# Optimization experiments

Measured on AMD Instinct MI355X. Metric: run time of the kernel, lower is better.

## Reference

```python
import math
import jax, jax.numpy as jnp
import numpy as np

WINDOW = (2, 7, 7)
SHIFT = (1, 3, 3)
NUM_HEADS = 4
DIM = 128
B, D, H, W = 1, 16, 112, 112  # divisible by window -> no padding, shift active


def _rel_coords_table():
    wd, wh, ww = WINDOW
    cd = np.arange(-(wd - 1), wd, dtype=np.float32)
    ch = np.arange(-(wh - 1), wh, dtype=np.float32)
    cw = np.arange(-(ww - 1), ww, dtype=np.float32)
    t = np.stack(np.meshgrid(cd, ch, cw, indexing='ij'), axis=-1)  # [2wd-1,2wh-1,2ww-1,3]
    t[..., 0] /= (wd - 1)
    t[..., 1] /= (wh - 1)
    t[..., 2] /= (ww - 1)
    t *= 8.0
    t = np.sign(t) * np.log2(np.abs(t) + 1.0) / 3.0
    return t.reshape(-1, 3)


def _rel_pos_index():
    wd, wh, ww = WINDOW
    coords = np.stack(np.meshgrid(np.arange(wd), np.arange(wh), np.arange(ww), indexing='ij'))
    cf = coords.reshape(3, -1)
    rc = (cf[:, :, None] - cf[:, None, :]).transpose(1, 2, 0)  # [N,N,3]
    rc[..., 0] += wd - 1
    rc[..., 1] += wh - 1
    rc[..., 2] += ww - 1
    rc[..., 0] *= (2 * wh - 1) * (2 * ww - 1)
    rc[..., 1] *= (2 * ww - 1)
    return rc.sum(-1).reshape(-1)


def _attn_mask(pd, ph, pw):
    wd, wh, ww = WINDOW
    sd, sh, sw = SHIFT
    m = np.zeros((pd, ph, pw), np.float32)
    cnt = 0
    for d in ((0, -wd), (-wd, -sd), (-sd, None)):
        for h in ((0, -wh), (-wh, -sh), (-sh, None)):
            for w in ((0, -ww), (-ww, -sw), (-sw, None)):
                m[d[0]:d[1], h[0]:h[1], w[0]:w[1]] = cnt
                cnt += 1
    nwin = (pd // wd) * (ph // wh) * (pw // ww)
    m = m.reshape(pd // wd, wd, ph // wh, wh, pw // ww, ww)
    m = m.transpose(0, 2, 4, 1, 3, 5).reshape(nwin, -1)  # [nWin, N]
    diff = m[:, None, :] - m[:, :, None]
    return np.where(diff != 0, -100.0, 0.0).astype(np.float32)


def setup_inputs() -> dict:
    key = jax.random.key(0)
    ks = jax.random.split(key, 5)
    C = DIM
    return {
        'x': jax.random.normal(ks[0], (B, D, H, W, C), jnp.float32),
        'qkv_weight': jax.random.normal(ks[1], (3 * C, C), jnp.float32) * 0.02,
        'qkv_bias': jnp.zeros((3 * C,), jnp.float32),
        'proj_weight': jax.random.normal(ks[2], (C, C), jnp.float32) * 0.02,
        'proj_bias': jnp.zeros((C,), jnp.float32),
        'logit_scale': jnp.full((NUM_HEADS, 1, 1), math.log(10.0), jnp.float32),
        'cpb_w1': jax.random.normal(ks[3], (512, 3), jnp.float32) * 0.02,
        'cpb_b1': jnp.zeros((512,), jnp.float32),
        'cpb_w2': jax.random.normal(ks[4], (NUM_HEADS, 512), jnp.float32) * 0.02,
    }


def reference(x, qkv_weight, qkv_bias, proj_weight, proj_bias, logit_scale, cpb_w1, cpb_b1, cpb_w2):
    wd, wh, ww = WINDOW
    sd, sh, sw = SHIFT
    b, d, h, w, C = x.shape
    N = wd * wh * ww
    hd = C // NUM_HEADS

    # --- continuous relative position bias (SwinV2) ---
    table = jnp.asarray(_rel_coords_table())              # [M, 3]
    hid = jax.nn.relu(table @ cpb_w1.T + cpb_b1)          # [M, 512]
    bias_tab = hid @ cpb_w2.T                             # [M, nH]
    idx = jnp.asarray(_rel_pos_index())                   # [N*N]
    rpb = bias_tab[idx].reshape(N, N, NUM_HEADS).transpose(2, 0, 1)
    rpb = 16.0 * jax.nn.sigmoid(rpb)                      # [nH, N, N]

    # zero middle third of qkv bias (cosine attention path)
    qkv_b = qkv_bias.at[C:2 * C].set(0.0)

    # --- shift + window partition (no padding: dims divisible) ---
    xs = jnp.roll(x, (-sd, -sh, -sw), axis=(1, 2, 3))
    nd, nh, nw = d // wd, h // wh, w // ww
    nwin = nd * nh * nw
    xw = xs.reshape(b, nd, wd, nh, wh, nw, ww, C)
    xw = xw.transpose(0, 1, 3, 5, 2, 4, 6, 7).reshape(b * nwin, N, C)

    # --- qkv + cosine attention ---
    qkv = (xw @ qkv_weight.T + qkv_b).reshape(b * nwin, N, 3, NUM_HEADS, hd)
    qkv = qkv.transpose(2, 0, 3, 1, 4)                    # [3, BW, nH, N, hd]
    q, k, v = qkv[0], qkv[1], qkv[2]
    qn = q / jnp.maximum(jnp.linalg.norm(q, axis=-1, keepdims=True), 1e-12)
    kn = k / jnp.maximum(jnp.linalg.norm(k, axis=-1, keepdims=True), 1e-12)
    attn = jnp.einsum('wnid,wnjd->wnij', qn, kn)          # [BW, nH, N, N]
    scale = jnp.exp(jnp.minimum(logit_scale, math.log(100.0)))  # [nH,1,1]
    attn = attn * scale[None] + rpb[None]

    # --- shift mask ---
    mask = jnp.asarray(_attn_mask(d, h, w))               # [nWin, N, N]
    attn = attn.reshape(b, nwin, NUM_HEADS, N, N) + mask[None, :, None]
    attn = jax.nn.softmax(attn.reshape(b * nwin, NUM_HEADS, N, N), axis=-1)

    out = jnp.einsum('wnij,wnjd->wind', attn, v).reshape(b * nwin, N, C)
    out = out @ proj_weight.T + proj_bias

    # --- reverse window partition + reverse shift ---
    out = out.reshape(b, nd, nh, nw, wd, wh, ww, C)
    out = out.transpose(0, 1, 4, 2, 5, 3, 6, 7).reshape(b, d, h, w, C)
    out = jnp.roll(out, (sd, sh, sw), axis=(1, 2, 3))
    return out
```

## Files before the change

kernel.cpp:

```cpp
#include <hip/hip_runtime.h>
#include <hip/hip_bf16.h>

typedef unsigned short u16;
typedef __attribute__((ext_vector_type(8))) short bf16x8;
typedef __attribute__((ext_vector_type(4))) float f32x4;

#define MFMA(a, b, c) __builtin_amdgcn_mfma_f32_16x16x32_bf16((a), (b), (c), 0, 0, 0)
#define LOG2E 1.4426950408889634f

__device__ __forceinline__ u16 f2b(float f) {
  __hip_bfloat16 h = __float2bfloat16(f);
  return __builtin_bit_cast(u16, h);
}
__device__ __forceinline__ float bu2f(u16 u) {
  union { unsigned u; float f; } v; v.u = ((unsigned)u) << 16; return v.f;
}
__device__ __forceinline__ u16 f2bu_sw(float f) {
  union { float f; unsigned u; } v; v.f = f;
  unsigned r = v.u + 0x7fffu + ((v.u >> 16) & 1u);
  return (u16)(r >> 16);
}
__device__ __forceinline__ int maskcode(int tok, int bd, int bh, int bw) {
  int d = tok / 49, rem = tok - d * 49, hh = rem / 7, w = rem - hh * 7;
  int rd = bd ? (d == 0 ? 1 : 2) : 0;
  int rh = bh ? (hh < 4 ? 1 : 2) : 0;
  int rw = bw ? (w < 4 ? 1 : 2) : 0;
  return rd * 9 + rh * 3 + rw;
}
__device__ __forceinline__ int tokbase(int tok, int id, int ih, int iw) {
  int d = tok / 49, rem = tok - d * 49, hh = rem / 7, w2 = rem - hh * 7;
  int pd = (id * 2 + d + 1) & 15;
  int ph = ih * 7 + hh + 3; if (ph >= 112) ph -= 112;
  int pw = iw * 7 + w2 + 3; if (pw >= 112) pw -= 112;
  return ((pd * 112 + ph) * 112 + pw) << 7;
}

__global__ void cpb_mlp(const float* __restrict__ w1, const float* __restrict__ b1,
                        const float* __restrict__ w2, float* __restrict__ btab) {
  const int m = blockIdx.x;
  const int k = threadIdx.x;
  const int i0 = m / 169, rm = m % 169, i1 = rm / 13, i2 = rm % 13;
  float c0 = (float)(i0 - 1) * 8.0f;
  float c1 = (float)(i1 - 6) * (8.0f / 6.0f);
  float c2 = (float)(i2 - 6) * (8.0f / 6.0f);
  float t0 = (c0 > 0.f ? 1.f : (c0 < 0.f ? -1.f : 0.f)) * log2f(fabsf(c0) + 1.f) * (1.f / 3.f);
  float t1 = (c1 > 0.f ? 1.f : (c1 < 0.f ? -1.f : 0.f)) * log2f(fabsf(c1) + 1.f) * (1.f / 3.f);
  float t2 = (c2 > 0.f ? 1.f : (c2 < 0.f ? -1.f : 0.f)) * log2f(fabsf(c2) + 1.f) * (1.f / 3.f);
  float hid = fmaxf(w1[k * 3 + 0] * t0 + w1[k * 3 + 1] * t1 + w1[k * 3 + 2] * t2 + b1[k], 0.f);
  __shared__ float red[4][8];
#pragma unroll
  for (int h = 0; h < 4; ++h) {
    float v = hid * w2[h * 512 + k];
    for (int mm = 1; mm < 64; mm <<= 1) v += __shfl_xor(v, mm);
    if ((k & 63) == 0) red[h][k >> 6] = v;
  }
  __syncthreads();
  if (k < 4) {
    float s = 0.f;
#pragma unroll
    for (int j = 0; j < 8; ++j) s += red[k][j];
    btab[m * 4 + k] = s;
  }
}

__global__ void build_rpbf(const float* __restrict__ btab, float* __restrict__ rpbf) {
  const int total = 8 * 4 * 7 * 7 * 64 * 4;
  int n = blockIdx.x * 256 + threadIdx.x;
  if (n >= total) return;
  int r = n & 3;
  int lane = (n >> 2) & 63;
  int q = n >> 8;
  int c = q % 7;
  int wv = (q / 7) % 7;
  int h = (q / 49) % 4;
  int combo = q / 196;
  int i = 16 * wv + (lane >> 4) * 4 + r;
  int j = 16 * c + (lane & 15);
  float v;
  if (j >= 98) {
    v = -1e30f;
  } else if (i >= 98) {
    v = 0.f;
  } else {
    int di = i / 49, ri = i % 49, hi_ = ri / 7, wi = ri % 7;
    int dj = j / 49, rj = j % 49, hj = rj / 7, wj = rj % 7;
    int idx = (di - dj + 1) * 169 + (hi_ - hj + 6) * 13 + (wi - wj + 6);
    float b = btab[idx * 4 + h];
    v = (16.f / (1.f + expf(-b))) * LOG2E;
    int bd = (combo >> 2) & 1, bh = (combo >> 1) & 1, bw = combo & 1;
    if (maskcode(i, bd, bh, bw) != maskcode(j, bd, bh, bw)) v -= 144.269504f;
  }
  rpbf[n] = v;
}

__global__ void pack_wqkv(const float* __restrict__ qkvw, u16* __restrict__ dst) {
  int bid = blockIdx.x;
  int h = bid / 160, rem = bid % 160, blk = rem / 32, r = rem % 32;
  int srow = (blk < 2 ? 0 : (blk < 4 ? 128 : 256)) + h * 32 + r;
  bool lo = (blk == 1) || (blk == 3);
  int c = threadIdx.x;
  float v = (c < 128) ? qkvw[srow * 128 + c] : 0.f;
  u16 hi = f2bu_sw(v);
  u16 outv = lo ? f2bu_sw(v - bu2f(hi)) : hi;
  dst[h * 21760 + blk * 4352 + r * 136 + c] = outv;
}

__global__ void pack_wproj(const float* __restrict__ pw, u16* __restrict__ dst) {
  int c = blockIdx.x;
  int m = threadIdx.x;
  float v = (m < 128) ? pw[c * 128 + m] : 0.f;
  dst[c * 136 + m] = f2bu_sw(v);
}

#define QHI 0
#define QLO 4480
#define KHI 8960
#define KLO 13440
#define VTB 14336
#define PIDX(i, t) ((i) * 128 + ((t) ^ (((i) & 7) << 3)))
#define VIDX(d, t) (VTB + (d) * 128 + ((t) ^ (((d) & 7) << 3)))

template <bool BF16OUT>
__global__ __launch_bounds__(448, 7) void swin_attn(
    const float* __restrict__ xg, const float* __restrict__ qkvb,
    const float* __restrict__ lscale, const float* __restrict__ rpbf,
    const u16* __restrict__ wqkv, u16* __restrict__ aoutb, float* __restrict__ aoutf) {
  __shared__ u16 lds[18432];
  const int tid = threadIdx.x;
  const int wv = tid >> 6;
  const int l = tid & 63;
  const int l15 = l & 15;
  const int lg = l >> 4;
  const int bid = blockIdx.x;
  const int win = ((bid >> 5) << 3) | (bid & 7);
  const int h = (bid >> 3) & 3;
  const int iw = win & 15, ih = (win >> 4) & 15, id = win >> 8;
  const int combo = ((id == 7) << 2) | ((ih == 15) << 1) | (iw == 15);

  {
    const uint4* src = (const uint4*)(wqkv + h * 21760);
    uint4* dst = (uint4*)lds;
    for (int it = tid; it < 2176; it += 448) dst[it] = src[it];
  }
  const int arow = 16 * wv + l15;
  bf16x8 xa[4];
  {
    const int base = tokbase((arow < 98) ? arow : 0, id, ih, iw);
    const float* xp = xg + base + lg * 8;
#pragma unroll
    for (int ks = 0; ks < 4; ++ks) {
      const float4 a = *(const float4*)(xp + ks * 32);
      const float4 b4 = *(const float4*)(xp + ks * 32 + 4);
      u16* xo = (u16*)&xa[ks];
      xo[0] = f2b(a.x); xo[1] = f2b(a.y); xo[2] = f2b(a.z); xo[3] = f2b(a.w);
      xo[4] = f2b(b4.x); xo[5] = f2b(b4.y); xo[6] = f2b(b4.z); xo[7] = f2b(b4.w);
    }
  }
  __syncthreads();

  const f32x4 zf = {0.f, 0.f, 0.f, 0.f};
  f32x4 aq0 = zf, aq1 = zf, ak0 = zf, ak1 = zf, av0 = zf, av1 = zf;
  const u16* wvb = wqkv + h * 21760 + 17408 + lg * 8;
  bf16x8 bv0 = *(const bf16x8*)(wvb + l15 * 136);
  bf16x8 bv1 = *(const bf16x8*)(wvb + (16 + l15) * 136);
  __builtin_amdgcn_s_setprio(1);
#pragma unroll
  for (int ks = 0; ks < 4; ++ks) {
    const int k0 = ks * 32 + lg * 8;
    bf16x8 nv0, nv1;
    if (ks < 3) {
      nv0 = *(const bf16x8*)(wvb + l15 * 136 + (ks + 1) * 32);
      nv1 = *(const bf16x8*)(wvb + (16 + l15) * 136 + (ks + 1) * 32);
    }
    bf16x8 b;
    b = *(const bf16x8*)(&lds[l15 * 136 + k0]);                aq0 = MFMA(xa[ks], b, aq0);
    b = *(const bf16x8*)(&lds[4352 + l15 * 136 + k0]);         aq0 = MFMA(xa[ks], b, aq0);
    b = *(const bf16x8*)(&lds[(16 + l15) * 136 + k0]);         aq1 = MFMA(xa[ks], b, aq1);
    b = *(const bf16x8*)(&lds[4352 + (16 + l15) * 136 + k0]);  aq1 = MFMA(xa[ks], b, aq1);
    b = *(const bf16x8*)(&lds[8704 + l15 * 136 + k0]);         ak0 = MFMA(xa[ks], b, ak0);
    b = *(const bf16x8*)(&lds[13056 + l15 * 136 + k0]);        ak0 = MFMA(xa[ks], b, ak0);
    b = *(const bf16x8*)(&lds[8704 + (16 + l15) * 136 + k0]);  ak1 = MFMA(xa[ks], b, ak1);
    b = *(const bf16x8*)(&lds[13056 + (16 + l15) * 136 + k0]); ak1 = MFMA(xa[ks], b, ak1);
    av0 = MFMA(xa[ks], bv0, av0);
    av1 = MFMA(xa[ks], bv1, av1);
    if (ks < 3) { bv0 = nv0; bv1 = nv1; }
  }
  __builtin_amdgcn_s_setprio(0);
  __syncthreads();

  const f32x4* rbf = (const f32x4*)rpbf + (((combo * 4 + h) * 7 + wv) * 7) * 64 + l;
  f32x4 att[7];
#pragma unroll
  for (int c = 0; c < 7; ++c) att[c] = rbf[c * 64];

  const float sc2 = __expf(fminf(lscale[h], 4.60517019f)) * LOG2E;
  const float qb0 = qkvb[h * 32 + l15];
  const float qb1 = qkvb[h * 32 + 16 + l15];
  const float vb0 = qkvb[256 + h * 32 + l15];
  const float vb1 = qkvb[256 + h * 32 + 16 + l15];
#pragma unroll
  for (int r = 0; r < 4; ++r) { aq0[r] += qb0; aq1[r] += qb1; av0[r] += vb0; av1[r] += vb1; }
#pragma unroll
  for (int r = 0; r < 4; ++r) {
    const int row = 16 * wv + lg * 4 + r;
    const bool ok = row < 98;
    float s = aq0[r] * aq0[r] + aq1[r] * aq1[r];
    s += __shfl_xor(s, 1); s += __shfl_xor(s, 2); s += __shfl_xor(s, 4); s += __shfl_xor(s, 8);
    float rn = sc2 * rsqrtf(fmaxf(s, 1e-24f));
    float q0 = ok ? aq0[r] * rn : 0.f, q1 = ok ? aq1[r] * rn : 0.f;
    u16 u0 = f2b(q0), u1 = f2b(q1);
    lds[QHI + row * 40 + l15] = u0;
    lds[QHI + row * 40 + 16 + l15] = u1;
    lds[QLO + row * 40 + l15] = f2b(q0 - bu2f(u0));
    lds[QLO + row * 40 + 16 + l15] = f2b(q1 - bu2f(u1));
    float sk = ak0[r] * ak0[r] + ak1[r] * ak1[r];
    sk += __shfl_xor(sk, 1); sk += __shfl_xor(sk, 2); sk += __shfl_xor(sk, 4); sk += __shfl_xor(sk, 8);
    float rk = rsqrtf(fmaxf(sk, 1e-24f));
    float k0v = ok ? ak0[r] * rk : 0.f, k1v = ok ? ak1[r] * rk : 0.f;
    u16 ku0 = f2b(k0v), ku1 = f2b(k1v);
    lds[KHI + row * 40 + l15] = ku0;
    lds[KHI + row * 40 + 16 + l15] = ku1;
    lds[KLO + row * 40 + l15] = f2b(k0v - bu2f(ku0));
    lds[KLO + row * 40 + 16 + l15] = f2b(k1v - bu2f(ku1));
  }
  __syncthreads();

  const bf16x8 qh = *(const bf16x8*)(&lds[QHI + (16 * wv + l15) * 40 + lg * 8]);
  const bf16x8 qlo = *(const bf16x8*)(&lds[QLO + (16 * wv + l15) * 40 + lg * 8]);
  __builtin_amdgcn_s_setprio(1);
#pragma unroll
  for (int c = 0; c < 7; ++c) {
    const bf16x8 kh = *(const bf16x8*)(&lds[KHI + (16 * c + l15) * 40 + lg * 8]);
    const bf16x8 kl = *(const bf16x8*)(&lds[KLO + (16 * c + l15) * 40 + lg * 8]);
    att[c] = MFMA(qh, kh, att[c]);
    att[c] = MFMA(qlo, kh, att[c]);
    att[c] = MFMA(qh, kl, att[c]);
  }
  __builtin_amdgcn_s_setprio(0);
  float rsv[4];
#pragma unroll
  for (int r = 0; r < 4; ++r) {
    float s = 0.f;
#pragma unroll
    for (int c = 0; c < 7; ++c) { float p = exp2f(att[c][r]); att[c][r] = p; s += p; }
    s += __shfl_xor(s, 1); s += __shfl_xor(s, 2); s += __shfl_xor(s, 4); s += __shfl_xor(s, 8);
    rsv[r] = 1.0f / s;
  }
  __syncthreads();

#pragma unroll
  for (int r = 0; r < 4; ++r) {
    const int i = 16 * wv + lg * 4 + r;
#pragma unroll
    for (int c = 0; c < 7; ++c) {
      const int t = 16 * c + l15;
      lds[PIDX(i, t)] = f2b(att[c][r] * rsv[r]);
    }
  }
  {
    const int t0 = 16 * wv + lg * 4;
    ushort4 v0, v1;
    v0.x = (t0 + 0 < 98) ? f2b(av0[0]) : (u16)0;
    v0.y = (t0 + 1 < 98) ? f2b(av0[1]) : (u16)0;
    v0.z = (t0 + 2 < 98) ? f2b(av0[2]) : (u16)0;
    v0.w = (t0 + 3 < 98) ? f2b(av0[3]) : (u16)0;
    v1.x = (t0 + 0 < 98) ? f2b(av1[0]) : (u16)0;
    v1.y = (t0 + 1 < 98) ? f2b(av1[1]) : (u16)0;
    v1.z = (t0 + 2 < 98) ? f2b(av1[2]) : (u16)0;
    v1.w = (t0 + 3 < 98) ? f2b(av1[3]) : (u16)0;
    *(ushort4*)(&lds[VIDX(l15, t0)]) = v0;
    *(ushort4*)(&lds[VIDX(16 + l15, t0)]) = v1;
  }
  for (int it = tid; it < 32 * 16; it += 448) {
    int dd = it >> 4, t = 112 + (it & 15);
    lds[VIDX(dd, t)] = 0;
  }
  __syncthreads();

  f32x4 o0 = zf, o1 = zf;
  __builtin_amdgcn_s_setprio(1);
#pragma unroll
  for (int ks = 0; ks < 4; ++ks) {
    const int t = ks * 32 + lg * 8;
    const bf16x8 pa = *(const bf16x8*)(&lds[PIDX(16 * wv + l15, t)]);
    const bf16x8 v0f = *(const bf16x8*)(&lds[VIDX(l15, t)]);
    const bf16x8 v1f = *(const bf16x8*)(&lds[VIDX(16 + l15, t)]);
    o0 = MFMA(v0f, pa, o0);
    o1 = MFMA(v1f, pa, o1);
  }
  __builtin_amdgcn_s_setprio(0);
  {
    const int tok = 16 * wv + l15;
    if (tok < 98) {
      if (BF16OUT) {
        u16* ab = aoutb + (win * 98 + tok) * 128 + h * 32;
        ushort4 s0, s1;
        s0.x = f2b(o0[0]); s0.y = f2b(o0[1]); s0.z = f2b(o0[2]); s0.w = f2b(o0[3]);
        s1.x = f2b(o1[0]); s1.y = f2b(o1[1]); s1.z = f2b(o1[2]); s1.w = f2b(o1[3]);
        *(ushort4*)(ab + lg * 4) = s0;
        *(ushort4*)(ab + 16 + lg * 4) = s1;
      } else {
        float* ab = aoutf + tokbase(tok, id, ih, iw) + h * 32;
        f32x4 s0 = o0, s1 = o1;
        *(f32x4*)(ab + lg * 4) = s0;
        *(f32x4*)(ab + 16 + lg * 4) = s1;
      }
    }
  }
}

template <bool BF16OUT>
__global__ __launch_bounds__(448, 7) void swin_proj(const u16* __restrict__ wp,
                                                    const float* __restrict__ projb,
                                                    const u16* __restrict__ aoutb,
                                                    float* io) {
  __shared__ u16 w[17408];
  __shared__ int tb[98];
  const int tid = threadIdx.x;
  const int wv = tid >> 6;
  const int l = tid & 63;
  const int l15 = l & 15;
  const int lg = l >> 4;
  const int win = blockIdx.x;
  const int iw = win & 15, ih = (win >> 4) & 15, id = win >> 8;
  if (tid < 98) tb[tid] = tokbase(tid, id, ih, iw);
  {
    const uint4* src = (const uint4*)wp;
    uint4* dst = (uint4*)w;
    for (int it = tid; it < 2176; it += 448) dst[it] = src[it];
  }
  __syncthreads();
  const int tok = 16 * wv + l15;
  const int tokc = (tok < 98) ? tok : 97;

  const f32x4 zf = {0.f, 0.f, 0.f, 0.f};
  f32x4 pr[8];
#pragma unroll
  for (int n = 0; n < 8; ++n) pr[n] = zf;
#pragma unroll
  for (int ks = 0; ks < 4; ++ks) {
    bf16x8 oa;
    if (BF16OUT) {
      oa = *(const bf16x8*)(aoutb + (win * 98 + tokc) * 128 + ks * 32 + lg * 8);
    } else {
      const float* ap = io + tb[tokc] + ks * 32 + lg * 8;
      const float4 f0 = *(const float4*)(ap);
      const float4 f1 = *(const float4*)(ap + 4);
      u16* op = (u16*)&oa;
      op[0] = f2b(f0.x); op[1] = f2b(f0.y); op[2] = f2b(f0.z); op[3] = f2b(f0.w);
      op[4] = f2b(f1.x); op[5] = f2b(f1.y); op[6] = f2b(f1.z); op[7] = f2b(f1.w);
    }
#pragma unroll
    for (int n = 0; n < 8; ++n) {
      const bf16x8 wbf = *(const bf16x8*)(&w[(16 * n + l15) * 136 + ks * 32 + lg * 8]);
      pr[n] = MFMA(wbf, oa, pr[n]);
    }
  }
#pragma unroll
  for (int n = 0; n < 8; ++n) {
    const float4 pb4 = *(const float4*)(projb + 16 * n + lg * 4);
    f32x4 o = pr[n];
    o[0] += pb4.x; o[1] += pb4.y; o[2] += pb4.z; o[3] += pb4.w;
    if (tok < 98) *(f32x4*)(io + tb[tok] + 16 * n + lg * 4) = o;
  }
}

extern "C" void kernel_launch(void* const* d_in, const int* in_sizes, int n_in,
                              void* d_out, int out_size, void* d_ws, size_t ws_size,
                              hipStream_t stream) {
  const float* xg = (const float*)d_in[0];
  const float* qkvw = (const float*)d_in[1];
  const float* qkvb = (const float*)d_in[2];
  const float* projw = (const float*)d_in[3];
  const float* projb = (const float*)d_in[4];
  const float* lsc = (const float*)d_in[5];
  const float* w1 = (const float*)d_in[6];
  const float* b1 = (const float*)d_in[7];
  const float* w2 = (const float*)d_in[8];

  char* ws = (char*)d_ws;
  float* btab = (float*)(ws);
  u16* wq = (u16*)(ws + 8192);
  u16* wp = (u16*)(ws + 182272);
  float* rpbf = (float*)(ws + 217088);
  u16* aoutb = (u16*)(ws + 1822720);
  float* io = (float*)d_out;

  const bool bf16path = ws_size >= (size_t)53202944;

  cpb_mlp<<<507, 512, 0, stream>>>(w1, b1, w2, btab);
  build_rpbf<<<(8 * 4 * 7 * 7 * 64 * 4 + 255) / 256, 256, 0, stream>>>(btab, rpbf);
  pack_wqkv<<<640, 136, 0, stream>>>(qkvw, wq);
  pack_wproj<<<128, 136, 0, stream>>>(projw, wp);
  if (bf16path) {
    swin_attn<true><<<8192, 448, 0, stream>>>(xg, qkvb, lsc, rpbf, wq, aoutb, io);
    swin_proj<true><<<2048, 448, 0, stream>>>(wp, projb, aoutb, io);
  } else {
    swin_attn<false><<<8192, 448, 0, stream>>>(xg, qkvb, lsc, rpbf, wq, nullptr, io);
    swin_proj<false><<<2048, 448, 0, stream>>>(wp, projb, nullptr, io);
  }
}
```

Before: 190.4 us.

## Transpose QK/score MFMA layout so per-token reductions stay in-lane

Swaps the MFMA operand order for the Q/K projection and the QK^T score product, so each lane holds one token's values across four registers instead of one value for each of four tokens. Row norms and the softmax sum then need only two cross-lane shuffles instead of four per row. The rel-pos table is rebuilt in the transposed order, Q/K/P go to LDS as vectorized ushort4 stores with an unswizzled padded P layout, and softmax normalization moves after the PV product onto the output. LDS use grows slightly, and the unswizzled P layout may add bank conflicts.

```diff
diff --git a/kernel.cpp b/kernel.cpp
--- a/kernel.cpp
+++ b/kernel.cpp
@@ -74,21 +74,21 @@
   int wv = (q / 7) % 7;
   int h = (q / 49) % 4;
   int combo = q / 196;
-  int i = 16 * wv + (lane >> 4) * 4 + r;
-  int j = 16 * c + (lane & 15);
+  int tokK = 16 * c + (lane >> 4) * 4 + r;
+  int tokQ = 16 * wv + (lane & 15);
   float v;
-  if (j >= 98) {
+  if (tokK >= 98) {
     v = -1e30f;
-  } else if (i >= 98) {
+  } else if (tokQ >= 98) {
     v = 0.f;
   } else {
-    int di = i / 49, ri = i % 49, hi_ = ri / 7, wi = ri % 7;
-    int dj = j / 49, rj = j % 49, hj = rj / 7, wj = rj % 7;
-    int idx = (di - dj + 1) * 169 + (hi_ - hj + 6) * 13 + (wi - wj + 6);
+    int dq = tokQ / 49, rq = tokQ % 49, hq = rq / 7, wq = rq % 7;
+    int dk = tokK / 49, rk = tokK % 49, hk = rk / 7, wk = rk % 7;
+    int idx = (dq - dk + 1) * 169 + (hq - hk + 6) * 13 + (wq - wk + 6);
     float b = btab[idx * 4 + h];
     v = (16.f / (1.f + expf(-b))) * LOG2E;
     int bd = (combo >> 2) & 1, bh = (combo >> 1) & 1, bw = combo & 1;
-    if (maskcode(i, bd, bh, bw) != maskcode(j, bd, bh, bw)) v -= 144.269504f;
+    if (maskcode(tokQ, bd, bh, bw) != maskcode(tokK, bd, bh, bw)) v -= 144.269504f;
   }
   rpbf[n] = v;
 }
@@ -116,8 +116,8 @@
 #define QLO 4480
 #define KHI 8960
 #define KLO 13440
-#define VTB 14336
-#define PIDX(i, t) ((i) * 128 + ((t) ^ (((i) & 7) << 3)))
+#define PB  0
+#define VTB 15232
 #define VIDX(d, t) (VTB + (d) * 128 + ((t) ^ (((d) & 7) << 3)))
 
 template <bool BF16OUT>
@@ -125,7 +125,7 @@
     const float* __restrict__ xg, const float* __restrict__ qkvb,
     const float* __restrict__ lscale, const float* __restrict__ rpbf,
     const u16* __restrict__ wqkv, u16* __restrict__ aoutb, float* __restrict__ aoutf) {
-  __shared__ u16 lds[18432];
+  __shared__ u16 lds[19328];
   const int tid = threadIdx.x;
   const int wv = tid >> 6;
   const int l = tid & 63;
@@ -173,14 +173,14 @@
       nv1 = *(const bf16x8*)(wvb + (16 + l15) * 136 + (ks + 1) * 32);
     }
     bf16x8 b;
-    b = *(const bf16x8*)(&lds[l15 * 136 + k0]);                aq0 = MFMA(xa[ks], b, aq0);
-    b = *(const bf16x8*)(&lds[4352 + l15 * 136 + k0]);         aq0 = MFMA(xa[ks], b, aq0);
-    b = *(const bf16x8*)(&lds[(16 + l15) * 136 + k0]);         aq1 = MFMA(xa[ks], b, aq1);
-    b = *(const bf16x8*)(&lds[4352 + (16 + l15) * 136 + k0]);  aq1 = MFMA(xa[ks], b, aq1);
-    b = *(const bf16x8*)(&lds[8704 + l15 * 136 + k0]);         ak0 = MFMA(xa[ks], b, ak0);
-    b = *(const bf16x8*)(&lds[13056 + l15 * 136 + k0]);        ak0 = MFMA(xa[ks], b, ak0);
-    b = *(const bf16x8*)(&lds[8704 + (16 + l15) * 136 + k0]);  ak1 = MFMA(xa[ks], b, ak1);
-    b = *(const bf16x8*)(&lds[13056 + (16 + l15) * 136 + k0]); ak1 = MFMA(xa[ks], b, ak1);
+    b = *(const bf16x8*)(&lds[l15 * 136 + k0]);                aq0 = MFMA(b, xa[ks], aq0);
+    b = *(const bf16x8*)(&lds[4352 + l15 * 136 + k0]);         aq0 = MFMA(b, xa[ks], aq0);
+    b = *(const bf16x8*)(&lds[(16 + l15) * 136 + k0]);         aq1 = MFMA(b, xa[ks], aq1);
+    b = *(const bf16x8*)(&lds[4352 + (16 + l15) * 136 + k0]);  aq1 = MFMA(b, xa[ks], aq1);
+    b = *(const bf16x8*)(&lds[8704 + l15 * 136 + k0]);         ak0 = MFMA(b, xa[ks], ak0);
+    b = *(const bf16x8*)(&lds[13056 + l15 * 136 + k0]);        ak0 = MFMA(b, xa[ks], ak0);
+    b = *(const bf16x8*)(&lds[8704 + (16 + l15) * 136 + k0]);  ak1 = MFMA(b, xa[ks], ak1);
+    b = *(const bf16x8*)(&lds[13056 + (16 + l15) * 136 + k0]); ak1 = MFMA(b, xa[ks], ak1);
     av0 = MFMA(xa[ks], bv0, av0);
     av1 = MFMA(xa[ks], bv1, av1);
     if (ks < 3) { bv0 = nv0; bv1 = nv1; }
@@ -194,68 +194,77 @@
   for (int c = 0; c < 7; ++c) att[c] = rbf[c * 64];
 
   const float sc2 = __expf(fminf(lscale[h], 4.60517019f)) * LOG2E;
-  const float qb0 = qkvb[h * 32 + l15];
-  const float qb1 = qkvb[h * 32 + 16 + l15];
+  const float4 qb0v = *(const float4*)(qkvb + h * 32 + lg * 4);
+  const float4 qb1v = *(const float4*)(qkvb + h * 32 + 16 + lg * 4);
   const float vb0 = qkvb[256 + h * 32 + l15];
   const float vb1 = qkvb[256 + h * 32 + 16 + l15];
-#pragma unroll
-  for (int r = 0; r < 4; ++r) { aq0[r] += qb0; aq1[r] += qb1; av0[r] += vb0; av1[r] += vb1; }
+  aq0[0] += qb0v.x; aq0[1] += qb0v.y; aq0[2] += qb0v.z; aq0[3] += qb0v.w;
+  aq1[0] += qb1v.x; aq1[1] += qb1v.y; aq1[2] += qb1v.z; aq1[3] += qb1v.w;
+#pragma unroll
+  for (int r = 0; r < 4; ++r) { av0[r] += vb0; av1[r] += vb1; }
+  float sq = 0.f, sk = 0.f;
 #pragma unroll
   for (int r = 0; r < 4; ++r) {
-    const int row = 16 * wv + lg * 4 + r;
-    const bool ok = row < 98;
-    float s = aq0[r] * aq0[r] + aq1[r] * aq1[r];
-    s += __shfl_xor(s, 1); s += __shfl_xor(s, 2); s += __shfl_xor(s, 4); s += __shfl_xor(s, 8);
-    float rn = sc2 * rsqrtf(fmaxf(s, 1e-24f));
-    float q0 = ok ? aq0[r] * rn : 0.f, q1 = ok ? aq1[r] * rn : 0.f;
-    u16 u0 = f2b(q0), u1 = f2b(q1);
-    lds[QHI + row * 40 + l15] = u0;
-    lds[QHI + row * 40 + 16 + l15] = u1;
-    lds[QLO + row * 40 + l15] = f2b(q0 - bu2f(u0));
-    lds[QLO + row * 40 + 16 + l15] = f2b(q1 - bu2f(u1));
-    float sk = ak0[r] * ak0[r] + ak1[r] * ak1[r];
-    sk += __shfl_xor(sk, 1); sk += __shfl_xor(sk, 2); sk += __shfl_xor(sk, 4); sk += __shfl_xor(sk, 8);
-    float rk = rsqrtf(fmaxf(sk, 1e-24f));
-    float k0v = ok ? ak0[r] * rk : 0.f, k1v = ok ? ak1[r] * rk : 0.f;
-    u16 ku0 = f2b(k0v), ku1 = f2b(k1v);
-    lds[KHI + row * 40 + l15] = ku0;
-    lds[KHI + row * 40 + 16 + l15] = ku1;
-    lds[KLO + row * 40 + l15] = f2b(k0v - bu2f(ku0));
-    lds[KLO + row * 40 + 16 + l15] = f2b(k1v - bu2f(ku1));
-  }
-  __syncthreads();
-
-  const bf16x8 qh = *(const bf16x8*)(&lds[QHI + (16 * wv + l15) * 40 + lg * 8]);
-  const bf16x8 qlo = *(const bf16x8*)(&lds[QLO + (16 * wv + l15) * 40 + lg * 8]);
+    sq += aq0[r] * aq0[r] + aq1[r] * aq1[r];
+    sk += ak0[r] * ak0[r] + ak1[r] * ak1[r];
+  }
+  sq += __shfl_xor(sq, 16); sq += __shfl_xor(sq, 32);
+  sk += __shfl_xor(sk, 16); sk += __shfl_xor(sk, 32);
+  const int tok = 16 * wv + l15;
+  const bool ok = tok < 98;
+  const float rnq = sc2 * rsqrtf(fmaxf(sq, 1e-24f));
+  const float rnk = rsqrtf(fmaxf(sk, 1e-24f));
+  {
+    ushort4 qh0, qh1, ql0, ql1, kh0, kh1, kl0, kl1;
+#pragma unroll
+    for (int r = 0; r < 4; ++r) {
+      float q0 = ok ? aq0[r] * rnq : 0.f;
+      float q1 = ok ? aq1[r] * rnq : 0.f;
+      float k0v = ok ? ak0[r] * rnk : 0.f;
+      float k1v = ok ? ak1[r] * rnk : 0.f;
+      u16 a = f2b(q0); ((u16*)&qh0)[r] = a; ((u16*)&ql0)[r] = f2b(q0 - bu2f(a));
+      u16 b2 = f2b(q1); ((u16*)&qh1)[r] = b2; ((u16*)&ql1)[r] = f2b(q1 - bu2f(b2));
+      u16 c2 = f2b(k0v); ((u16*)&kh0)[r] = c2; ((u16*)&kl0)[r] = f2b(k0v - bu2f(c2));
+      u16 d2 = f2b(k1v); ((u16*)&kh1)[r] = d2; ((u16*)&kl1)[r] = f2b(k1v - bu2f(d2));
+    }
+    *(ushort4*)(&lds[QHI + tok * 40 + lg * 4]) = qh0;
+    *(ushort4*)(&lds[QHI + tok * 40 + 16 + lg * 4]) = qh1;
+    *(ushort4*)(&lds[QLO + tok * 40 + lg * 4]) = ql0;
+    *(ushort4*)(&lds[QLO + tok * 40 + 16 + lg * 4]) = ql1;
+    *(ushort4*)(&lds[KHI + tok * 40 + lg * 4]) = kh0;
+    *(ushort4*)(&lds[KHI + tok * 40 + 16 + lg * 4]) = kh1;
+    *(ushort4*)(&lds[KLO + tok * 40 + lg * 4]) = kl0;
+    *(ushort4*)(&lds[KLO + tok * 40 + 16 + lg * 4]) = kl1;
+  }
+  __syncthreads();
+
+  const bf16x8 qh = *(const bf16x8*)(&lds[QHI + tok * 40 + lg * 8]);
+  const bf16x8 qlo = *(const bf16x8*)(&lds[QLO + tok * 40 + lg * 8]);
   __builtin_amdgcn_s_setprio(1);
 #pragma unroll
   for (int c = 0; c < 7; ++c) {
     const bf16x8 kh = *(const bf16x8*)(&lds[KHI + (16 * c + l15) * 40 + lg * 8]);
     const bf16x8 kl = *(const bf16x8*)(&lds[KLO + (16 * c + l15) * 40 + lg * 8]);
-    att[c] = MFMA(qh, kh, att[c]);
-    att[c] = MFMA(qlo, kh, att[c]);
-    att[c] = MFMA(qh, kl, att[c]);
+    att[c] = MFMA(kh, qh, att[c]);
+    att[c] = MFMA(kh, qlo, att[c]);
+    att[c] = MFMA(kl, qh, att[c]);
   }
   __builtin_amdgcn_s_setprio(0);
-  float rsv[4];
-#pragma unroll
-  for (int r = 0; r < 4; ++r) {
-    float s = 0.f;
-#pragma unroll
-    for (int c = 0; c < 7; ++c) { float p = exp2f(att[c][r]); att[c][r] = p; s += p; }
-    s += __shfl_xor(s, 1); s += __shfl_xor(s, 2); s += __shfl_xor(s, 4); s += __shfl_xor(s, 8);
-    rsv[r] = 1.0f / s;
-  }
-  __syncthreads();
-
-#pragma unroll
-  for (int r = 0; r < 4; ++r) {
-    const int i = 16 * wv + lg * 4 + r;
-#pragma unroll
-    for (int c = 0; c < 7; ++c) {
-      const int t = 16 * c + l15;
-      lds[PIDX(i, t)] = f2b(att[c][r] * rsv[r]);
-    }
+  float s = 0.f;
+#pragma unroll
+  for (int c = 0; c < 7; ++c)
+#pragma unroll
+    for (int r = 0; r < 4; ++r) { float p = exp2f(att[c][r]); att[c][r] = p; s += p; }
+  s += __shfl_xor(s, 16); s += __shfl_xor(s, 32);
+  const float rsv = 1.0f / s;
+  __syncthreads();
+
+#pragma unroll
+  for (int c = 0; c < 7; ++c) {
+    ushort4 pk;
+#pragma unroll
+    for (int r = 0; r < 4; ++r) ((u16*)&pk)[r] = ok ? f2b(att[c][r]) : (u16)0;
+    *(ushort4*)(&lds[PB + tok * 136 + 16 * c + lg * 4]) = pk;
   }
   {
     const int t0 = 16 * wv + lg * 4;
@@ -282,29 +291,30 @@
 #pragma unroll
   for (int ks = 0; ks < 4; ++ks) {
     const int t = ks * 32 + lg * 8;
-    const bf16x8 pa = *(const bf16x8*)(&lds[PIDX(16 * wv + l15, t)]);
+    const bf16x8 pb = *(const bf16x8*)(&lds[PB + tok * 136 + t]);
     const bf16x8 v0f = *(const bf16x8*)(&lds[VIDX(l15, t)]);
     const bf16x8 v1f = *(const bf16x8*)(&lds[VIDX(16 + l15, t)]);
-    o0 = MFMA(v0f, pa, o0);
-    o1 = MFMA(v1f, pa, o1);
+    o0 = MFMA(v0f, pb, o0);
+    o1 = MFMA(v1f, pb, o1);
   }
   __builtin_amdgcn_s_setprio(0);
-  {
-    const int tok = 16 * wv + l15;
-    if (tok < 98) {
-      if (BF16OUT) {
-        u16* ab = aoutb + (win * 98 + tok) * 128 + h * 32;
-        ushort4 s0, s1;
-        s0.x = f2b(o0[0]); s0.y = f2b(o0[1]); s0.z = f2b(o0[2]); s0.w = f2b(o0[3]);
-        s1.x = f2b(o1[0]); s1.y = f2b(o1[1]); s1.z = f2b(o1[2]); s1.w = f2b(o1[3]);
-        *(ushort4*)(ab + lg * 4) = s0;
-        *(ushort4*)(ab + 16 + lg * 4) = s1;
-      } else {
-        float* ab = aoutf + tokbase(tok, id, ih, iw) + h * 32;
-        f32x4 s0 = o0, s1 = o1;
-        *(f32x4*)(ab + lg * 4) = s0;
-        *(f32x4*)(ab + 16 + lg * 4) = s1;
-      }
+  if (ok) {
+    if (BF16OUT) {
+      u16* ab = aoutb + (win * 98 + tok) * 128 + h * 32;
+      ushort4 s0, s1;
+      s0.x = f2b(o0[0] * rsv); s0.y = f2b(o0[1] * rsv);
+      s0.z = f2b(o0[2] * rsv); s0.w = f2b(o0[3] * rsv);
+      s1.x = f2b(o1[0] * rsv); s1.y = f2b(o1[1] * rsv);
+      s1.z = f2b(o1[2] * rsv); s1.w = f2b(o1[3] * rsv);
+      *(ushort4*)(ab + lg * 4) = s0;
+      *(ushort4*)(ab + 16 + lg * 4) = s1;
+    } else {
+      float* ab = aoutf + tokbase(tok, id, ih, iw) + h * 32;
+      f32x4 s0, s1;
+#pragma unroll
+      for (int r = 0; r < 4; ++r) { s0[r] = o0[r] * rsv; s1[r] = o1[r] * rsv; }
+      *(f32x4*)(ab + lg * 4) = s0;
+      *(f32x4*)(ab + 16 + lg * 4) = s1;
     }
   }
 }
```

Measured after the change: 179.6 us. 1.06x faster.
